# Kernel tuning notes

Measured on AMD Instinct MI355X. Metric: run time of the kernel, lower is better.

Reference implementation:

```python
import jax, jax.numpy as jnp
import numpy as np

C = 256
CI = C // 2  # inter_channels


def conv1x1(x, w, b):
    # x: [B,C,H,W], w: [O,C], b: [O] -> [B,O,H,W]
    return jnp.einsum('bchw,oc->bohw', x, w) + b[None, :, None, None]


def setup_inputs() -> dict:
    key = jax.random.key(0)
    ks = jax.random.split(key, 9)
    B, H, W = 8, 56, 56
    s = 0.02
    return {
        'x': jax.random.normal(ks[0], (B, C, H, W), dtype=jnp.float32),
        'g_w': jax.random.normal(ks[1], (CI, C), dtype=jnp.float32) * s,
        'g_b': jax.random.normal(ks[2], (CI,), dtype=jnp.float32) * s,
        'theta_w': jax.random.normal(ks[3], (CI, C), dtype=jnp.float32) * s,
        'theta_b': jax.random.normal(ks[4], (CI,), dtype=jnp.float32) * s,
        'phi_w': jax.random.normal(ks[5], (CI, C), dtype=jnp.float32) * s,
        'phi_b': jax.random.normal(ks[6], (CI,), dtype=jnp.float32) * s,
        'W_w': jax.random.normal(ks[7], (C, CI), dtype=jnp.float32) * s,
        'W_b': jax.random.normal(ks[8], (C,), dtype=jnp.float32) * s,
    }


def reference(x, g_w, g_b, theta_w, theta_b, phi_w, phi_b, W_w, W_b):
    B, Cc, H, Wd = x.shape
    N = H * Wd
    g_x = conv1x1(x, g_w, g_b).reshape(B, CI, N).transpose(0, 2, 1)        # [B,N,CI]
    theta_x = conv1x1(x, theta_w, theta_b).reshape(B, CI, N).transpose(0, 2, 1)  # [B,N,CI]
    phi_x = conv1x1(x, phi_w, phi_b).reshape(B, CI, N)                     # [B,CI,N]
    f = jnp.einsum('bnc,bcm->bnm', theta_x, phi_x)                         # [B,N,N]
    attn = jax.nn.softmax(f, axis=-1)
    y = jnp.einsum('bnm,bmc->bnc', attn, g_x)                              # [B,N,CI]
    y = y.transpose(0, 2, 1).reshape(B, CI, H, Wd)                         # [B,CI,H,W]
    z = conv1x1(y, W_w, W_b) + x
    return z
```

## Files before the change

kernel.cpp:

```cpp
#include <hip/hip_runtime.h>

#define NB 8
#define C 256
#define CI 128
#define NPIX 3136
#define NT 64
#define NTILES 49
#define NSPLIT 4

typedef unsigned short u16;
typedef unsigned int u32;
typedef __bf16 bf16x8 __attribute__((ext_vector_type(8)));
typedef float f32x4 __attribute__((ext_vector_type(4)));

static __device__ __forceinline__ u16 f2b(float f) {
  union { float f; u32 u; } v; v.f = f;
  u32 r = v.u + 0x7FFFu + ((v.u >> 16) & 1u);
  return (u16)(r >> 16);
}
static __device__ __forceinline__ float b2f(u16 v) {
  union { u32 u; float f; } x; x.u = ((u32)v) << 16; return x.f;
}
static __device__ __forceinline__ u32 cvtpk(float lo, float hi) {
  u32 r;
  asm("v_cvt_pk_bf16_f32 %0, %1, %2" : "=v"(r) : "v"(lo), "v"(hi));
  return r;
}
static __device__ __forceinline__ void plswap(u32& x, u32& y) {
  asm("v_permlane32_swap_b32 %0, %1" : "+v"(x), "+v"(y));
  asm("v_permlane16_swap_b32 %0, %1" : "+v"(x), "+v"(y));
}
static __device__ __forceinline__ void gl16(const void* g, void* l) {
  __builtin_amdgcn_global_load_lds(
      (const __attribute__((address_space(1))) u32*)g,
      (__attribute__((address_space(3))) u32*)l, 16, 0, 0);
}

__global__ __launch_bounds__(256) void k0_convert(
    const float* __restrict__ g_w, const float* __restrict__ th_w,
    const float* __restrict__ ph_w, const float* __restrict__ W_w,
    u16* __restrict__ wcat, u16* __restrict__ Wbf) {
  int i = blockIdx.x * 256 + threadIdx.x;
  if (i < 98304) {
    int o = i >> 8, c = i & 255;
    float v = (o < 128) ? g_w[o * 256 + c]
            : (o < 256) ? th_w[(o - 128) * 256 + c]
                        : ph_w[(o - 256) * 256 + c];
    wcat[i] = f2b(v);
  } else {
    int j = i - 98304;
    Wbf[j] = f2b(W_w[j]);
  }
}

__global__ __launch_bounds__(256) void k1_proj(
    const float* __restrict__ x, const float* __restrict__ g_b,
    const float* __restrict__ th_b, const float* __restrict__ ph_b,
    const u16* __restrict__ wcat, u16* __restrict__ thO,
    u16* __restrict__ phO, u16* __restrict__ gO) {
  __shared__ __align__(16) u16 xT[64 * 256];
  char* xTb = reinterpret_cast<char*>(xT);
  int tid = threadIdx.x;
  int b = blockIdx.x / NTILES, nt = blockIdx.x % NTILES;
  int n0 = nt * NT;
  const float* xb = x + (size_t)b * C * NPIX;
  {
    int c0 = tid >> 4, nq = tid & 15;
    for (int k = 0; k < 16; ++k) {
      int c = c0 + 16 * k;
      float4 xv = *reinterpret_cast<const float4*>(xb + (size_t)c * NPIX + n0 + 4 * nq);
      float vals[4] = {xv.x, xv.y, xv.z, xv.w};
#pragma unroll
      for (int j = 0; j < 4; ++j) {
        int row = 4 * nq + j;
        int off = row * 512 + ((((c >> 3) ^ (row & 7))) << 4) + (c & 7) * 2;
        *reinterpret_cast<u16*>(xTb + off) = f2b(vals[j]);
      }
    }
  }
  __syncthreads();
  int wave = tid >> 6, lane = tid & 63;
  int r = 16 * wave + (lane & 15);
  bf16x8 a[8];
#pragma unroll
  for (int kk = 0; kk < 8; ++kk) {
    int ch = 4 * kk + (lane >> 4);
    a[kk] = *reinterpret_cast<const bf16x8*>(xTb + r * 512 + ((ch ^ (r & 7)) << 4));
  }
  for (int os = 0; os < 24; ++os) {
    int o = 16 * os + (lane & 15);
    f32x4 acc = {0.f, 0.f, 0.f, 0.f};
    const u16* wrow = wcat + (size_t)o * 256 + 8 * (lane >> 4);
#pragma unroll
    for (int kk = 0; kk < 8; ++kk) {
      bf16x8 bb = *reinterpret_cast<const bf16x8*>(wrow + 32 * kk);
      acc = __builtin_amdgcn_mfma_f32_16x16x32_bf16(a[kk], bb, acc, 0, 0, 0);
    }
    int p = os >> 3;
    int ol = (os & 7) * 16 + (lane & 15);
    const float* bias = (p == 0) ? g_b : (p == 1) ? th_b : ph_b;
    float bv = bias[ol];
    int nbase = n0 + 16 * wave + 4 * (lane >> 4);
    if (p == 0) {
      ushort4 pk;
      pk.x = f2b(acc[0] + bv); pk.y = f2b(acc[1] + bv);
      pk.z = f2b(acc[2] + bv); pk.w = f2b(acc[3] + bv);
      *reinterpret_cast<ushort4*>(gO + ((size_t)b * CI + ol) * NPIX + nbase) = pk;
    } else {
      u16* dst = (p == 1) ? thO : phO;
#pragma unroll
      for (int j = 0; j < 4; ++j)
        dst[((size_t)b * NPIX + nbase + j) * CI + ol] = f2b(acc[j] + bv);
    }
  }
}

__global__ __launch_bounds__(256) void k2_attn(
    const u16* __restrict__ th, const u16* __restrict__ ph,
    const u16* __restrict__ gbuf, u16* __restrict__ yp,
    float* __restrict__ lm) {
  __shared__ __align__(16) char lds[65536];
  int tid = threadIdx.x, wave = tid >> 6, lane = tid & 63;
  int h = lane >> 4, q = lane & 15;
  int bid = blockIdx.x;
  int s = bid & 3, rest = bid >> 2;
  int b = rest / NTILES, nt = rest % NTILES;
  int n0 = nt * NT;
  int ts = (NTILES * s) >> 2, te = (NTILES * (s + 1)) >> 2;

  bf16x8 bth[4];
  {
    const u16* trow = th + ((size_t)b * NPIX + n0 + 16 * wave + q) * CI;
#pragma unroll
    for (int kk = 0; kk < 4; ++kk)
      bth[kk] = *reinterpret_cast<const bf16x8*>(trow + 32 * kk + 8 * h);
  }
  float mrun = -1e30f, lrun = 0.f;
  f32x4 yacc[8];
#pragma unroll
  for (int cs = 0; cs < 8; ++cs) yacc[cs] = {0.f, 0.f, 0.f, 0.f};

  auto stage = [&](int buf, int mt) {
    int m0 = mt * NT;
    char* phB = lds + buf * 16384;
    char* gB = lds + 32768 + buf * 16384;
#pragma unroll
    for (int c = 0; c < 4; ++c) {
      int call = wave * 4 + c;
      int o = call * 1024 + lane * 16;
      int row = o >> 8, chl = (o >> 4) & 15;
      int chg = chl ^ (row & 7);
      gl16(ph + ((size_t)(b * NPIX + m0 + row)) * CI + chg * 8, phB + call * 1024);
    }
#pragma unroll
    for (int c = 0; c < 4; ++c) {
      int call = wave * 4 + c;
      int o = call * 1024 + lane * 16;
      int ci = o >> 7, chl = (o >> 4) & 7;
      int chg = chl ^ (ci & 7);
      gl16(gbuf + ((size_t)b * CI + ci) * NPIX + m0 + chg * 8, gB + call * 1024);
    }
  };

  stage(0, ts);
  __syncthreads();
  int cur = 0;
  for (int mt = ts; mt < te; ++mt) {
    if (mt + 1 < te) stage(cur ^ 1, mt + 1);
    char* phB = lds + cur * 16384;
    char* gB = lds + 32768 + cur * 16384;
    f32x4 sv[4];
#pragma unroll
    for (int ms = 0; ms < 4; ++ms) {
      sv[ms] = {0.f, 0.f, 0.f, 0.f};
      int mr = 16 * ms + q;
      int rb = mr * 256, sw = (mr & 7) << 4;
#pragma unroll
      for (int kk = 0; kk < 4; ++kk) {
        bf16x8 av = *reinterpret_cast<const bf16x8*>(phB + rb + (((4 * kk + h) << 4) ^ sw));
        sv[ms] = __builtin_amdgcn_mfma_f32_16x16x32_bf16(av, bth[kk], sv[ms], 0, 0, 0);
      }
    }
    float pmax = sv[0][0];
#pragma unroll
    for (int ms = 0; ms < 4; ++ms)
#pragma unroll
      for (int j = 0; j < 4; ++j) pmax = fmaxf(pmax, sv[ms][j]);
    pmax = fmaxf(pmax, __shfl_xor(pmax, 16));
    pmax = fmaxf(pmax, __shfl_xor(pmax, 32));
    if (!__all(pmax <= mrun + 8.f)) {
      float mn = fmaxf(mrun, pmax);
      float corr = __expf(mrun - mn);
      mrun = mn; lrun *= corr;
      float cr[4];
#pragma unroll
      for (int j = 0; j < 4; ++j) cr[j] = __shfl(corr, 4 * h + j);
#pragma unroll
      for (int cs = 0; cs < 8; ++cs)
#pragma unroll
        for (int j = 0; j < 4; ++j) yacc[cs][j] *= cr[j];
    }
    float pe[4][4];
    float rs = 0.f;
#pragma unroll
    for (int ms = 0; ms < 4; ++ms)
#pragma unroll
      for (int j = 0; j < 4; ++j) {
        pe[ms][j] = __expf(sv[ms][j] - mrun);
        rs += pe[ms][j];
      }
    rs += __shfl_xor(rs, 16);
    rs += __shfl_xor(rs, 32);
    lrun += rs;
#pragma unroll
    for (int kk = 0; kk < 2; ++kk) {
      u32 x0 = cvtpk(pe[2 * kk][0], pe[2 * kk][1]);
      u32 x1 = cvtpk(pe[2 * kk][2], pe[2 * kk][3]);
      u32 y0 = cvtpk(pe[2 * kk + 1][0], pe[2 * kk + 1][1]);
      u32 y1 = cvtpk(pe[2 * kk + 1][2], pe[2 * kk + 1][3]);
      plswap(x0, y0);
      plswap(x1, y1);
      union { u32 u[4]; bf16x8 v; } f;
      f.u[0] = x0; f.u[1] = x1; f.u[2] = y0; f.u[3] = y1;
#pragma unroll
      for (int cs = 0; cs < 8; ++cs) {
        int ci = 16 * cs + q;
        bf16x8 gv = *reinterpret_cast<const bf16x8*>(
            gB + ci * 128 + ((((4 * kk + h)) ^ (ci & 7)) << 4));
        yacc[cs] = __builtin_amdgcn_mfma_f32_16x16x32_bf16(f.v, gv, yacc[cs], 0, 0, 0);
      }
    }
    __syncthreads();
    cur ^= 1;
  }
  u16* ypb = yp + (size_t)(s * NB + b) * NPIX * CI;
#pragma unroll
  for (int cs = 0; cs < 8; ++cs)
#pragma unroll
    for (int j = 0; j < 4; ++j) {
      int n = n0 + 16 * wave + 4 * h + j;
      ypb[(size_t)n * CI + 16 * cs + q] = f2b(yacc[cs][j]);
    }
  if (h == 0) {
    int n = n0 + 16 * wave + q;
    float* lmb = lm + (size_t)(s * NB + b) * 2 * NPIX;
    lmb[n] = mrun;
    lmb[NPIX + n] = lrun;
  }
}

__global__ __launch_bounds__(256) void k3_out(
    const u16* __restrict__ yp, const float* __restrict__ lm,
    const u16* __restrict__ Wbf, const float* __restrict__ W_b,
    const float* __restrict__ x, float* __restrict__ z) {
  __shared__ __align__(16) u16 yT[64 * 128];
  char* yTb = reinterpret_cast<char*>(yT);
  int tid = threadIdx.x, wave = tid >> 6, lane = tid & 63;
  int b = blockIdx.x / NTILES, nt = blockIdx.x % NTILES;
  int n0 = nt * NT;
#pragma unroll
  for (int i = 0; i < 4; ++i) {
    int qq = tid + i * 256;
    int row = qq >> 4, ch = qq & 15;
    int n = n0 + row;
    float mv[NSPLIT], lv[NSPLIT];
    float M = -1e30f;
#pragma unroll
    for (int s = 0; s < NSPLIT; ++s) {
      const float* lmb = lm + (size_t)(s * NB + b) * 2 * NPIX;
      mv[s] = lmb[n]; lv[s] = lmb[NPIX + n];
      M = fmaxf(M, mv[s]);
    }
    float num[8];
#pragma unroll
    for (int e = 0; e < 8; ++e) num[e] = 0.f;
    float den = 0.f;
#pragma unroll
    for (int s = 0; s < NSPLIT; ++s) {
      float w = __expf(mv[s] - M);
      den += w * lv[s];
      union { uint4 u4; u16 us[8]; } yv;
      yv.u4 = *reinterpret_cast<const uint4*>(
          yp + (size_t)(s * NB + b) * NPIX * CI + (size_t)n * CI + ch * 8);
#pragma unroll
      for (int e = 0; e < 8; ++e) num[e] += w * b2f(yv.us[e]);
    }
    float inv = 1.f / den;
    union { uint4 u4; u16 us[8]; } ov;
#pragma unroll
    for (int e = 0; e < 8; ++e) ov.us[e] = f2b(num[e] * inv);
    *reinterpret_cast<uint4*>(yTb + row * 256 + ((ch ^ (row & 7)) << 4)) = ov.u4;
  }
  __syncthreads();
  bf16x8 a[4];
  int r = 16 * wave + (lane & 15);
#pragma unroll
  for (int kk = 0; kk < 4; ++kk) {
    int ch = 4 * kk + (lane >> 4);
    a[kk] = *reinterpret_cast<const bf16x8*>(yTb + r * 256 + ((ch ^ (r & 7)) << 4));
  }
  for (int os = 0; os < 16; ++os) {
    int co = 16 * os + (lane & 15);
    f32x4 acc = {0.f, 0.f, 0.f, 0.f};
    const u16* wrow = Wbf + (size_t)co * 128 + 8 * (lane >> 4);
#pragma unroll
    for (int kk = 0; kk < 4; ++kk) {
      bf16x8 bb = *reinterpret_cast<const bf16x8*>(wrow + 32 * kk);
      acc = __builtin_amdgcn_mfma_f32_16x16x32_bf16(a[kk], bb, acc, 0, 0, 0);
    }
    float bw = W_b[co];
    int nb = n0 + 16 * wave + 4 * (lane >> 4);
    size_t off = ((size_t)b * C + co) * NPIX + nb;
    float4 xv = *reinterpret_cast<const float4*>(x + off);
    float4 o;
    o.x = acc[0] + bw + xv.x; o.y = acc[1] + bw + xv.y;
    o.z = acc[2] + bw + xv.z; o.w = acc[3] + bw + xv.w;
    *reinterpret_cast<float4*>(z + off) = o;
  }
}

extern "C" void kernel_launch(void* const* d_in, const int* in_sizes, int n_in,
                              void* d_out, int out_size, void* d_ws, size_t ws_size,
                              hipStream_t stream) {
  const float* x    = (const float*)d_in[0];
  const float* g_w  = (const float*)d_in[1];
  const float* g_b  = (const float*)d_in[2];
  const float* th_w = (const float*)d_in[3];
  const float* th_b = (const float*)d_in[4];
  const float* ph_w = (const float*)d_in[5];
  const float* ph_b = (const float*)d_in[6];
  const float* W_w  = (const float*)d_in[7];
  const float* W_b  = (const float*)d_in[8];
  float* z = (float*)d_out;
  u16* ws = (u16*)d_ws;
  u16* wcat = ws;
  u16* Wbf  = ws + 98304;
  u16* th   = ws + 131072;
  u16* phb  = th + 3211264;
  u16* gbb  = phb + 3211264;
  u16* yp   = gbb + 3211264;
  float* lm = (float*)(ws + 131072 + (size_t)3211264 * 7);
  hipLaunchKernelGGL(k0_convert, dim3(512), dim3(256), 0, stream,
                     g_w, th_w, ph_w, W_w, wcat, Wbf);
  hipLaunchKernelGGL(k1_proj, dim3(NB * NTILES), dim3(256), 0, stream,
                     x, g_b, th_b, ph_b, wcat, th, phb, gbb);
  hipLaunchKernelGGL(k2_attn, dim3(NB * NTILES * NSPLIT), dim3(256), 0, stream,
                     th, phb, gbb, yp, lm);
  hipLaunchKernelGGL(k3_out, dim3(NB * NTILES), dim3(256), 0, stream,
                     yp, lm, Wbf, W_b, x, z);
}
```

Before: 167.2 us.

## Use 32x32 MFMA tiles with 128-query blocks and exp2 softmax in attention

Restructures the attention kernel so each wave owns 32 query rows with 32x32x16 MFMAs, and each block covers 128 queries. This doubles reuse of the staged phi/g tiles per LDS load and halves the block count. LOG2E is folded into the theta weights and bias so the softmax can use exp2 directly, and the rescale threshold is widened. The last group overlaps the previous one to handle the ragged edge, recomputing some rows. It also adds setprio hints and a launch-bounds occupancy hint, at the cost of higher register pressure.

```diff
diff --git a/kernel.cpp b/kernel.cpp
--- a/kernel.cpp
+++ b/kernel.cpp
@@ -6,12 +6,15 @@
 #define NPIX 3136
 #define NT 64
 #define NTILES 49
+#define NG 25
 #define NSPLIT 4
+#define LOG2E 1.44269504f
 
 typedef unsigned short u16;
 typedef unsigned int u32;
 typedef __bf16 bf16x8 __attribute__((ext_vector_type(8)));
 typedef float f32x4 __attribute__((ext_vector_type(4)));
+typedef float f32x16 __attribute__((ext_vector_type(16)));
 
 static __device__ __forceinline__ u16 f2b(float f) {
   union { float f; u32 u; } v; v.f = f;
@@ -26,9 +29,8 @@
   asm("v_cvt_pk_bf16_f32 %0, %1, %2" : "=v"(r) : "v"(lo), "v"(hi));
   return r;
 }
-static __device__ __forceinline__ void plswap(u32& x, u32& y) {
+static __device__ __forceinline__ void swap32(u32& x, u32& y) {
   asm("v_permlane32_swap_b32 %0, %1" : "+v"(x), "+v"(y));
-  asm("v_permlane16_swap_b32 %0, %1" : "+v"(x), "+v"(y));
 }
 static __device__ __forceinline__ void gl16(const void* g, void* l) {
   __builtin_amdgcn_global_load_lds(
@@ -44,7 +46,7 @@
   if (i < 98304) {
     int o = i >> 8, c = i & 255;
     float v = (o < 128) ? g_w[o * 256 + c]
-            : (o < 256) ? th_w[(o - 128) * 256 + c]
+            : (o < 256) ? th_w[(o - 128) * 256 + c] * LOG2E
                         : ph_w[(o - 256) * 256 + c];
     wcat[i] = f2b(v);
   } else {
@@ -100,6 +102,7 @@
     int ol = (os & 7) * 16 + (lane & 15);
     const float* bias = (p == 0) ? g_b : (p == 1) ? th_b : ph_b;
     float bv = bias[ol];
+    if (p == 1) bv *= LOG2E;
     int nbase = n0 + 16 * wave + 4 * (lane >> 4);
     if (p == 0) {
       ushort4 pk;
@@ -115,30 +118,33 @@
   }
 }
 
-__global__ __launch_bounds__(256) void k2_attn(
+__global__ __launch_bounds__(256, 2) void k2_attn(
     const u16* __restrict__ th, const u16* __restrict__ ph,
     const u16* __restrict__ gbuf, u16* __restrict__ yp,
     float* __restrict__ lm) {
   __shared__ __align__(16) char lds[65536];
   int tid = threadIdx.x, wave = tid >> 6, lane = tid & 63;
-  int h = lane >> 4, q = lane & 15;
+  int h5 = lane >> 5, l31 = lane & 31;
   int bid = blockIdx.x;
   int s = bid & 3, rest = bid >> 2;
-  int b = rest / NTILES, nt = rest % NTILES;
-  int n0 = nt * NT;
+  int b = rest / NG, ng = rest % NG;
+  int qbase = ng * 128 + wave * 32;
+  if (qbase + 32 > NPIX) qbase -= 64;
   int ts = (NTILES * s) >> 2, te = (NTILES * (s + 1)) >> 2;
 
-  bf16x8 bth[4];
+  bf16x8 bth[8];
   {
-    const u16* trow = th + ((size_t)b * NPIX + n0 + 16 * wave + q) * CI;
-#pragma unroll
-    for (int kk = 0; kk < 4; ++kk)
-      bth[kk] = *reinterpret_cast<const bf16x8*>(trow + 32 * kk + 8 * h);
+    const u16* trow = th + ((size_t)b * NPIX + qbase + l31) * CI;
+#pragma unroll
+    for (int ks = 0; ks < 8; ++ks)
+      bth[ks] = *reinterpret_cast<const bf16x8*>(trow + 16 * ks + 8 * h5);
   }
   float mrun = -1e30f, lrun = 0.f;
-  f32x4 yacc[8];
-#pragma unroll
-  for (int cs = 0; cs < 8; ++cs) yacc[cs] = {0.f, 0.f, 0.f, 0.f};
+  f32x16 yacc[4];
+#pragma unroll
+  for (int cb = 0; cb < 4; ++cb)
+#pragma unroll
+    for (int j = 0; j < 16; ++j) yacc[cb][j] = 0.f;
 
   auto stage = [&](int buf, int mt) {
     int m0 = mt * NT;
@@ -169,80 +175,98 @@
     if (mt + 1 < te) stage(cur ^ 1, mt + 1);
     char* phB = lds + cur * 16384;
     char* gB = lds + 32768 + cur * 16384;
-    f32x4 sv[4];
-#pragma unroll
-    for (int ms = 0; ms < 4; ++ms) {
-      sv[ms] = {0.f, 0.f, 0.f, 0.f};
-      int mr = 16 * ms + q;
-      int rb = mr * 256, sw = (mr & 7) << 4;
-#pragma unroll
-      for (int kk = 0; kk < 4; ++kk) {
-        bf16x8 av = *reinterpret_cast<const bf16x8*>(phB + rb + (((4 * kk + h) << 4) ^ sw));
-        sv[ms] = __builtin_amdgcn_mfma_f32_16x16x32_bf16(av, bth[kk], sv[ms], 0, 0, 0);
+    f32x16 sv0, sv1;
+#pragma unroll
+    for (int j = 0; j < 16; ++j) { sv0[j] = 0.f; sv1[j] = 0.f; }
+    __builtin_amdgcn_s_setprio(1);
+#pragma unroll
+    for (int ks = 0; ks < 8; ++ks) {
+      int chk = 2 * ks + h5;
+      int off = l31 * 256 + ((chk ^ (l31 & 7)) << 4);
+      bf16x8 a0 = *reinterpret_cast<const bf16x8*>(phB + off);
+      bf16x8 a1 = *reinterpret_cast<const bf16x8*>(phB + off + 8192);
+      sv0 = __builtin_amdgcn_mfma_f32_32x32x16_bf16(a0, bth[ks], sv0, 0, 0, 0);
+      sv1 = __builtin_amdgcn_mfma_f32_32x32x16_bf16(a1, bth[ks], sv1, 0, 0, 0);
+    }
+    __builtin_amdgcn_s_setprio(0);
+    float m8[8];
+#pragma unroll
+    for (int i = 0; i < 8; ++i)
+      m8[i] = fmaxf(fmaxf(sv0[i], sv0[i + 8]), fmaxf(sv1[i], sv1[i + 8]));
+    float pmax = fmaxf(fmaxf(fmaxf(m8[0], m8[1]), fmaxf(m8[2], m8[3])),
+                       fmaxf(fmaxf(m8[4], m8[5]), fmaxf(m8[6], m8[7])));
+    pmax = fmaxf(pmax, __shfl_xor(pmax, 32));
+    if (!__all(pmax <= mrun + 11.5f)) {
+      float mn = fmaxf(mrun, pmax);
+      float corr = exp2f(mrun - mn);
+      mrun = mn; lrun *= corr;
+      float cr[16];
+#pragma unroll
+      for (int j = 0; j < 16; ++j) {
+        int row = (j & 3) + 8 * (j >> 2) + 4 * h5;
+        cr[j] = __shfl(corr, row + 32 * h5);
       }
-    }
-    float pmax = sv[0][0];
-#pragma unroll
-    for (int ms = 0; ms < 4; ++ms)
-#pragma unroll
-      for (int j = 0; j < 4; ++j) pmax = fmaxf(pmax, sv[ms][j]);
-    pmax = fmaxf(pmax, __shfl_xor(pmax, 16));
-    pmax = fmaxf(pmax, __shfl_xor(pmax, 32));
-    if (!__all(pmax <= mrun + 8.f)) {
-      float mn = fmaxf(mrun, pmax);
-      float corr = __expf(mrun - mn);
-      mrun = mn; lrun *= corr;
-      float cr[4];
-#pragma unroll
-      for (int j = 0; j < 4; ++j) cr[j] = __shfl(corr, 4 * h + j);
-#pragma unroll
-      for (int cs = 0; cs < 8; ++cs)
-#pragma unroll
-        for (int j = 0; j < 4; ++j) yacc[cs][j] *= cr[j];
-    }
-    float pe[4][4];
-    float rs = 0.f;
-#pragma unroll
-    for (int ms = 0; ms < 4; ++ms)
-#pragma unroll
-      for (int j = 0; j < 4; ++j) {
-        pe[ms][j] = __expf(sv[ms][j] - mrun);
-        rs += pe[ms][j];
-      }
-    rs += __shfl_xor(rs, 16);
+#pragma unroll
+      for (int cb = 0; cb < 4; ++cb)
+#pragma unroll
+        for (int j = 0; j < 16; ++j) yacc[cb][j] *= cr[j];
+    }
+#pragma unroll
+    for (int j = 0; j < 16; ++j) {
+      sv0[j] = exp2f(sv0[j] - mrun);
+      sv1[j] = exp2f(sv1[j] - mrun);
+    }
+    float a0 = 0.f, a1 = 0.f, a2 = 0.f, a3 = 0.f;
+#pragma unroll
+    for (int i = 0; i < 16; i += 4) {
+      a0 += sv0[i] + sv1[i];
+      a1 += sv0[i + 1] + sv1[i + 1];
+      a2 += sv0[i + 2] + sv1[i + 2];
+      a3 += sv0[i + 3] + sv1[i + 3];
+    }
+    float rs = (a0 + a1) + (a2 + a3);
     rs += __shfl_xor(rs, 32);
     lrun += rs;
-#pragma unroll
-    for (int kk = 0; kk < 2; ++kk) {
-      u32 x0 = cvtpk(pe[2 * kk][0], pe[2 * kk][1]);
-      u32 x1 = cvtpk(pe[2 * kk][2], pe[2 * kk][3]);
-      u32 y0 = cvtpk(pe[2 * kk + 1][0], pe[2 * kk + 1][1]);
-      u32 y1 = cvtpk(pe[2 * kk + 1][2], pe[2 * kk + 1][3]);
-      plswap(x0, y0);
-      plswap(x1, y1);
+    u32 pk[2][4][2];
+#pragma unroll
+    for (int t = 0; t < 4; ++t) {
+      pk[0][t][0] = cvtpk(sv0[4 * t], sv0[4 * t + 1]);
+      pk[0][t][1] = cvtpk(sv0[4 * t + 2], sv0[4 * t + 3]);
+      pk[1][t][0] = cvtpk(sv1[4 * t], sv1[4 * t + 1]);
+      pk[1][t][1] = cvtpk(sv1[4 * t + 2], sv1[4 * t + 3]);
+    }
+    __builtin_amdgcn_s_setprio(1);
+#pragma unroll
+    for (int ks = 0; ks < 4; ++ks) {
+      int m2 = ks >> 1, t0 = 2 * (ks & 1);
+      swap32(pk[m2][t0][0], pk[m2][t0 + 1][0]);
+      swap32(pk[m2][t0][1], pk[m2][t0 + 1][1]);
       union { u32 u[4]; bf16x8 v; } f;
-      f.u[0] = x0; f.u[1] = x1; f.u[2] = y0; f.u[3] = y1;
-#pragma unroll
-      for (int cs = 0; cs < 8; ++cs) {
-        int ci = 16 * cs + q;
+      f.u[0] = pk[m2][t0][0]; f.u[1] = pk[m2][t0][1];
+      f.u[2] = pk[m2][t0 + 1][0]; f.u[3] = pk[m2][t0 + 1][1];
+      int chk = 2 * ks + h5;
+#pragma unroll
+      for (int cb = 0; cb < 4; ++cb) {
+        int ci = 32 * cb + l31;
         bf16x8 gv = *reinterpret_cast<const bf16x8*>(
-            gB + ci * 128 + ((((4 * kk + h)) ^ (ci & 7)) << 4));
-        yacc[cs] = __builtin_amdgcn_mfma_f32_16x16x32_bf16(f.v, gv, yacc[cs], 0, 0, 0);
+            gB + ci * 128 + ((chk ^ (ci & 7)) << 4));
+        yacc[cb] = __builtin_amdgcn_mfma_f32_32x32x16_bf16(f.v, gv, yacc[cb], 0, 0, 0);
       }
     }
+    __builtin_amdgcn_s_setprio(0);
     __syncthreads();
     cur ^= 1;
   }
   u16* ypb = yp + (size_t)(s * NB + b) * NPIX * CI;
 #pragma unroll
-  for (int cs = 0; cs < 8; ++cs)
-#pragma unroll
-    for (int j = 0; j < 4; ++j) {
-      int n = n0 + 16 * wave + 4 * h + j;
-      ypb[(size_t)n * CI + 16 * cs + q] = f2b(yacc[cs][j]);
-    }
-  if (h == 0) {
-    int n = n0 + 16 * wave + q;
+  for (int cb = 0; cb < 4; ++cb)
+#pragma unroll
+    for (int j = 0; j < 16; ++j) {
+      int n = qbase + (j & 3) + 8 * (j >> 2) + 4 * h5;
+      ypb[(size_t)n * CI + 32 * cb + l31] = f2b(yacc[cb][j]);
+    }
+  if (lane < 32) {
+    int n = qbase + l31;
     float* lmb = lm + (size_t)(s * NB + b) * 2 * NPIX;
     lmb[n] = mrun;
     lmb[NPIX + n] = lrun;
@@ -277,7 +301,7 @@
     float den = 0.f;
 #pragma unroll
     for (int s = 0; s < NSPLIT; ++s) {
-      float w = __expf(mv[s] - M);
+      float w = exp2f(mv[s] - M);
       den += w * lv[s];
       union { uint4 u4; u16 us[8]; } yv;
       yv.u4 = *reinterpret_cast<const uint4*>(
@@ -344,7 +368,7 @@
                      g_w, th_w, ph_w, W_w, wcat, Wbf);
   hipLaunchKernelGGL(k1_proj, dim3(NB * NTILES), dim3(256), 0, stream,
                      x, g_b, th_b, ph_b, wcat, th, phb, gbb);
-  hipLaunchKernelGGL(k2_attn, dim3(NB * NTILES * NSPLIT), dim3(256), 0, stream,
+  hipLaunchKernelGGL(k2_attn, dim3(NB * NG * NSPLIT), dim3(256), 0, stream,
                      th, phb, gbb, yp, lm);
   hipLaunchKernelGGL(k3_out, dim3(NB * NTILES), dim3(256), 0, stream,
                      yp, lm, Wbf, W_b, x, z);
```

New measurement: 157.2 us. 6.0% less time.
